# Kernel optimization log

Hardware: AMD Instinct MI355X
Metric: run time of the kernel (lower is better)

## Reference

```python
import jax, jax.numpy as jnp
import numpy as np

NUM_NODES = 100000
NUM_EDGES = 1600000
NUM_GRAPHS = 64
D_IN = 128
HID = 256
N_ATTR = 8
D_OUT = 1


def setup_inputs() -> dict:
    key = jax.random.key(0)
    ks = jax.random.split(key, 16)
    x = jax.random.normal(ks[0], (NUM_NODES, D_IN), dtype=jnp.float32)
    edge_index = jax.random.randint(ks[1], (2, NUM_EDGES), 0, NUM_NODES, dtype=jnp.int64)
    batch = jnp.sort(jax.random.randint(ks[2], (NUM_NODES,), 0, NUM_GRAPHS, dtype=jnp.int64))
    graph_attr = jax.random.normal(ks[3], (NUM_GRAPHS, N_ATTR), dtype=jnp.float32)
    def lin(k, fi, fo):
        s = 1.0 / np.sqrt(fi)
        return jax.random.uniform(k, (fi, fo), jnp.float32, -s, s)
    # SAGEConv: lin_l (applied to aggregated neighbors, has bias) + lin_r (root, no bias)
    W1l = lin(ks[4], D_IN, HID); b1 = jnp.zeros((HID,), jnp.float32)
    W1r = lin(ks[5], D_IN, HID)
    W2l = lin(ks[6], HID, HID); b2 = jnp.zeros((HID,), jnp.float32)
    W2r = lin(ks[7], HID, HID)
    Wf1 = lin(ks[8], HID + N_ATTR, HID); bf1 = jnp.zeros((HID,), jnp.float32)
    Wf2 = lin(ks[9], HID, D_OUT); bf2 = jnp.zeros((D_OUT,), jnp.float32)
    return {"x": x, "edge_index": edge_index, "batch": batch, "graph_attr": graph_attr,
            "W1l": W1l, "b1": b1, "W1r": W1r, "W2l": W2l, "b2": b2, "W2r": W2r,
            "Wf1": Wf1, "bf1": bf1, "Wf2": Wf2, "bf2": bf2}


def _mean_agg(h, src, dst, num_segments):
    # gather source features, scatter-mean into destination nodes
    s = jax.ops.segment_sum(h[src], dst, num_segments=num_segments)
    cnt = jax.ops.segment_sum(jnp.ones((src.shape[0], 1), h.dtype), dst, num_segments=num_segments)
    return s / jnp.maximum(cnt, 1.0)


def _sage(h, src, dst, Wl, b, Wr):
    agg = _mean_agg(h, src, dst, h.shape[0])
    return agg @ Wl + b + h @ Wr


def reference(x, edge_index, batch, graph_attr, W1l, b1, W1r, W2l, b2, W2r, Wf1, bf1, Wf2, bf2):
    src, dst = edge_index[0], edge_index[1]
    h = jax.nn.relu(_sage(x, src, dst, W1l, b1, W1r))
    h = _sage(h, src, dst, W2l, b2, W2r)
    # global mean pool over graphs
    gsum = jax.ops.segment_sum(h, batch, num_segments=NUM_GRAPHS)
    gcnt = jax.ops.segment_sum(jnp.ones((h.shape[0], 1), h.dtype), batch, num_segments=NUM_GRAPHS)
    g = gsum / jnp.maximum(gcnt, 1.0)
    g = jnp.concatenate([g, graph_attr.reshape(-1, N_ATTR)], axis=1)
    g = jax.nn.relu(g @ Wf1 + bf1)
    return g @ Wf2 + bf2
```

## Files before the change

### kernel.cpp

```cpp
#include <hip/hip_runtime.h>
#include <stdint.h>

#define NN 100000
#define NE 1600000
#define NG 64
#define DIN 128
#define HID 256
#define NATTR 8
#define NBK 391
#define CAP 6144
#define PCH 4096
#define BWW 25000
#define CB 12756
#define AEL 2048

typedef unsigned short u16;
typedef __attribute__((ext_vector_type(8))) short s16x8;
typedef __attribute__((ext_vector_type(4))) float f32x4;
typedef __attribute__((ext_vector_type(2))) float f32x2;

__device__ __forceinline__ int imaxi(int a, int b) { return a > b ? a : b; }
__device__ __forceinline__ u16 f2bf(float f) {
    unsigned u = __float_as_uint(f);
    return (u16)((u + 0x7fffu + ((u >> 16) & 1u)) >> 16);
}
__device__ __forceinline__ void gload16(const void* g, void* l) {
    __builtin_amdgcn_global_load_lds((const __attribute__((address_space(1))) void*)g,
                                     (__attribute__((address_space(3))) void*)l, 16, 0, 0);
}


__global__ void k_prep(const float4* __restrict__ x4, ushort4* __restrict__ xb4,
                       const float* __restrict__ W1l, const float* __restrict__ W1r,
                       u16* __restrict__ W1lt, u16* __restrict__ W1rt,
                       float4* __restrict__ P84, const int* __restrict__ batch,
                       int* __restrict__ goff, int* __restrict__ gcnt,
                       int* __restrict__ cursor) {
    int b = blockIdx.x, t = threadIdx.x;
    if (b < CB) {
        int i = b * 256 + t;
        const int NX4 = NN * DIN / 4;
        if (i < NX4) {
            float4 v = x4[i];
            ushort4 o;
            o.x = f2bf(v.x); o.y = f2bf(v.y); o.z = f2bf(v.z); o.w = f2bf(v.w);
            xb4[i] = o;
        } else {
            int j = i - NX4;
            if (j < 32768) {
                int n = j >> 7, k = j & 127;
                W1lt[j] = f2bf(W1l[k * HID + n]);
            } else if (j < 65536) {
                int jj = j - 32768;
                int n = jj >> 7, k = jj & 127;
                W1rt[jj] = f2bf(W1r[k * HID + n]);
            }
        }
    } else if (b < CB + 256) {
        int i = (b - CB) * 256 + t;
        P84[i] = make_float4(0.f, 0.f, 0.f, 0.f);
    } else {
        for (int i = t; i < NBK; i += 256) cursor[i] = 0;
        int g = t;
        if (g <= NG) {
            int lo = 0, hi = NN;
            while (lo < hi) {
                int mid = (lo + hi) >> 1;
                if (batch[mid] < g) lo = mid + 1; else hi = mid;
            }
            goff[g] = lo;
        }
        __syncthreads();
        if (g < NG) gcnt[g] = goff[g + 1] - goff[g];
    }
}


__global__ __launch_bounds__(256) void k_part(const int* __restrict__ ei,
                                              int* __restrict__ cursor,
                                              unsigned* __restrict__ pairs) {
    __shared__ unsigned spk[PCH];
    __shared__ unsigned short sbk[PCH];
    __shared__ int hist[NBK], gb[NBK];
    __shared__ int sc[512];
    int t = threadIdx.x;
    int c0 = blockIdx.x * PCH;
    int n = NE - c0; if (n > PCH) n = PCH;
    for (int i = t; i < NBK; i += 256) hist[i] = 0;
    __syncthreads();
    unsigned mypk[16]; unsigned short mybk[16]; int myoff[16];
#pragma unroll
    for (int j = 0; j < 16; j++) {
        int i = t + j * 256;
        myoff[j] = -1;
        if (i < n) {
            int e = c0 + i;
            unsigned d = (unsigned)__builtin_nontemporal_load(&ei[NE + e]);
            unsigned s = (unsigned)__builtin_nontemporal_load(&ei[e]);
            unsigned bk = d >> 8;
            mypk[j] = ((d & 255u) << 24) | s;
            mybk[j] = (unsigned short)bk;
            myoff[j] = atomicAdd(&hist[bk], 1);
        }
    }
    __syncthreads();
    sc[t] = (t < NBK) ? hist[t] : 0;
    sc[t + 256] = (t + 256 < NBK) ? hist[t + 256] : 0;
    __syncthreads();
    for (int off = 1; off < 512; off <<= 1) {
        int v0 = (t >= off) ? sc[t - off] : 0;
        int v1 = (t + 256 >= off) ? sc[t + 256 - off] : 0;
        __syncthreads();
        sc[t] += v0; sc[t + 256] += v1;
        __syncthreads();
    }
    if (t < NBK && hist[t] > 0) gb[t] = atomicAdd(&cursor[t], hist[t]);
    if (t + 256 < NBK && hist[t + 256] > 0)
        gb[t + 256] = atomicAdd(&cursor[t + 256], hist[t + 256]);
    __syncthreads();
#pragma unroll
    for (int j = 0; j < 16; j++) {
        if (myoff[j] >= 0) {
            int bk = mybk[j];
            int pos = sc[bk] - hist[bk] + myoff[j];
            spk[pos] = mypk[j];
            sbk[pos] = (unsigned short)bk;
        }
    }
    __syncthreads();
    for (int i = t; i < n; i += 256) {
        int bk = sbk[i];
        int local = gb[bk] + (i - (sc[bk] - hist[bk]));
        pairs[(size_t)bk * CAP + local] = spk[i];
    }
}


__global__ __launch_bounds__(256) void k_csr(const unsigned* __restrict__ pairs,
                                             const int* __restrict__ cursor,
                                             int* __restrict__ rowptr,
                                             unsigned* __restrict__ col) {
    __shared__ unsigned colL[CAP];
    __shared__ int csc[512];
    __shared__ int cnt[256], cur[256], sc[256];
    int b = blockIdx.x, t = threadIdx.x;
    csc[t] = (t < NBK) ? cursor[t] : 0;
    csc[t + 256] = (t + 256 < NBK) ? cursor[t + 256] : 0;
    __syncthreads();
    for (int off = 1; off < 512; off <<= 1) {
        int v0 = (t >= off) ? csc[t - off] : 0;
        int v1 = (t + 256 >= off) ? csc[t + 256 - off] : 0;
        __syncthreads();
        csc[t] += v0; csc[t + 256] += v1;
        __syncthreads();
    }
    int obase = (b == 0) ? 0 : csc[b - 1];
    int ecnt = cursor[b];
    const unsigned* pp = pairs + (size_t)b * CAP;
    cnt[t] = 0;
    __syncthreads();
    for (int i = t; i < ecnt; i += 256)
        atomicAdd(&cnt[pp[i] >> 24], 1);
    __syncthreads();
    sc[t] = cnt[t];
    __syncthreads();
    for (int off = 1; off < 256; off <<= 1) {
        int v = (t >= off) ? sc[t - off] : 0;
        __syncthreads();
        sc[t] += v;
        __syncthreads();
    }
    int lr = sc[t] - cnt[t];
    cur[t] = lr;
    int node = (b << 8) + t;
    if (node < NN) rowptr[node] = obase + lr;
    if (b == NBK - 1 && t == 0) rowptr[NN] = obase + ecnt;
    __syncthreads();
    for (int i = t; i < ecnt; i += 256) {
        unsigned p = pp[i];
        int dl = p >> 24;
        int pos = atomicAdd(&cur[dl], 1);
        int dd = cnt[dl]; if (dd > 32767) dd = 32767;
        colL[pos] = ((unsigned)dd << 17) | (p & 0xFFFFFFu);
    }
    __syncthreads();
    for (int i = t; i < ecnt; i += 256)
        col[obase + i] = colL[i];
}


__global__ __launch_bounds__(256, 8) void k_agg(const uint4* __restrict__ xb4,
                                                uint4* __restrict__ agg4,
                                                const int* __restrict__ rowptr,
                                                const unsigned* __restrict__ col,
                                                int node0) {
    __shared__ unsigned scol[AEL];
    int t = threadIdx.x;
    int base = node0 + blockIdx.x * 16;
    int wave = t >> 6, lane = t & 63;
    int qtr = lane >> 4, li = lane & 15;
    int node = base + (wave << 2) + qtr;
    int s = rowptr[node], e = rowptr[node + 1];
    int bs = rowptr[base], be = rowptr[base + 16];
    int bn = be - bs;
    bool inl = bn <= AEL;
    if (inl)
        for (int j = t; j < bn; j += 256) scol[j] = col[bs + j];
    __syncthreads();

    f32x2 b01 = {0.f, 0.f}, b23 = {0.f, 0.f}, b45 = {0.f, 0.f}, b67 = {0.f, 0.f};
    const uint4* xp = xb4 + li;

#define ACC8(V) do { \
        f32x2 p; \
        p[0] = __uint_as_float((V).x << 16); p[1] = __uint_as_float((V).x & 0xffff0000u); b01 += p; \
        p[0] = __uint_as_float((V).y << 16); p[1] = __uint_as_float((V).y & 0xffff0000u); b23 += p; \
        p[0] = __uint_as_float((V).z << 16); p[1] = __uint_as_float((V).z & 0xffff0000u); b45 += p; \
        p[0] = __uint_as_float((V).w << 16); p[1] = __uint_as_float((V).w & 0xffff0000u); b67 += p; \
    } while (0)

#define CL(X) scol[(X) - bs]
#define CG(X) col[X]
#define AGG_BODY(CIDX) do { \
        for (; i + 8 <= e; i += 8) { \
            unsigned c0 = (CIDX(i + 0)) & 0x1FFFFu; \
            unsigned c1 = (CIDX(i + 1)) & 0x1FFFFu; \
            unsigned c2 = (CIDX(i + 2)) & 0x1FFFFu; \
            unsigned c3 = (CIDX(i + 3)) & 0x1FFFFu; \
            unsigned c4 = (CIDX(i + 4)) & 0x1FFFFu; \
            unsigned c5 = (CIDX(i + 5)) & 0x1FFFFu; \
            unsigned c6 = (CIDX(i + 6)) & 0x1FFFFu; \
            unsigned c7 = (CIDX(i + 7)) & 0x1FFFFu; \
            uint4 w0 = xp[(size_t)c0 * 16]; \
            uint4 w1 = xp[(size_t)c1 * 16]; \
            uint4 w2 = xp[(size_t)c2 * 16]; \
            uint4 w3 = xp[(size_t)c3 * 16]; \
            uint4 w4 = xp[(size_t)c4 * 16]; \
            uint4 w5 = xp[(size_t)c5 * 16]; \
            uint4 w6 = xp[(size_t)c6 * 16]; \
            uint4 w7 = xp[(size_t)c7 * 16]; \
            ACC8(w0); ACC8(w1); ACC8(w2); ACC8(w3); \
            ACC8(w4); ACC8(w5); ACC8(w6); ACC8(w7); \
        } \
        for (; i + 2 <= e; i += 2) { \
            unsigned c0 = (CIDX(i + 0)) & 0x1FFFFu; \
            unsigned c1 = (CIDX(i + 1)) & 0x1FFFFu; \
            uint4 w0 = xp[(size_t)c0 * 16]; \
            uint4 w1 = xp[(size_t)c1 * 16]; \
            ACC8(w0); ACC8(w1); \
        } \
        if (i < e) { \
            unsigned c0 = (CIDX(i)) & 0x1FFFFu; \
            uint4 w0 = xp[(size_t)c0 * 16]; \
            ACC8(w0); \
        } \
    } while (0)

    int i = s;
    if (inl) { AGG_BODY(CL); } else { AGG_BODY(CG); }
#undef AGG_BODY
#undef CL
#undef CG
#undef ACC8

    float inv = 1.f / (float)imaxi(e - s, 1);
    uint4 o;
    o.x = (((unsigned)f2bf(b01[1] * inv)) << 16) | (unsigned)f2bf(b01[0] * inv);
    o.y = (((unsigned)f2bf(b23[1] * inv)) << 16) | (unsigned)f2bf(b23[0] * inv);
    o.z = (((unsigned)f2bf(b45[1] * inv)) << 16) | (unsigned)f2bf(b45[0] * inv);
    o.w = (((unsigned)f2bf(b67[1] * inv)) << 16) | (unsigned)f2bf(b67[0] * inv);
    agg4[(size_t)node * 16 + li] = o;
}


__global__ __launch_bounds__(512) void k_gemm1(
    const u16* __restrict__ agg1, const u16* __restrict__ xb,
    const u16* __restrict__ W1lt, const u16* __restrict__ W1rt,
    const float* __restrict__ b1, u16* __restrict__ h1t) {
    __shared__ u16 As[128][32];
    __shared__ u16 Bs[256][32];
    int t = threadIdx.x;
    int m0 = blockIdx.x * 128;
    int wave = t >> 6, lane = t & 63;
    int wm = wave & 1, wn = wave >> 1;
    int lm = lane & 15, quad = lane >> 4;
    int ar = t >> 2, aq = t & 3;
    f32x4 acc[4][4] = {};
    const u16* Ap = agg1;
    const u16* Bp = W1lt;
#pragma unroll
    for (int ph = 0; ph < 2; ph++) {
        for (int k0 = 0; k0 < DIN; k0 += 32) {
            gload16(Ap + (size_t)(m0 + ar) * DIN + k0 + aq * 8, &As[wave * 16][0]);
#pragma unroll
            for (int i = 0; i < 2; i++) {
                int r = (t + i * 512) >> 2;
                gload16(Bp + (size_t)r * DIN + k0 + aq * 8, &Bs[wave * 16 + i * 128][0]);
            }
            __syncthreads();
            s16x8 af[4], bfr[4];
#pragma unroll
            for (int i = 0; i < 4; i++) {
                af[i]  = *(const s16x8*)&As[wm * 64 + i * 16 + lm][quad * 8];
                bfr[i] = *(const s16x8*)&Bs[wn * 64 + i * 16 + lm][quad * 8];
            }
#pragma unroll
            for (int mi = 0; mi < 4; mi++)
#pragma unroll
                for (int ni = 0; ni < 4; ni++)
                    acc[mi][ni] = __builtin_amdgcn_mfma_f32_16x16x32_bf16(
                        af[mi], bfr[ni], acc[mi][ni], 0, 0, 0);
            __syncthreads();
        }
        Ap = xb; Bp = W1rt;
    }
#pragma unroll
    for (int ni = 0; ni < 4; ni++) {
        int colf = wn * 64 + ni * 16 + lm;
        float bias = b1[colf];
#pragma unroll
        for (int mi = 0; mi < 4; mi++) {
            int row = m0 + wm * 64 + mi * 16 + quad * 4;
            if (row < NN) {
                ushort4 o;
                o.x = f2bf(fmaxf(acc[mi][ni][0] + bias, 0.f));
                o.y = f2bf(fmaxf(acc[mi][ni][1] + bias, 0.f));
                o.z = f2bf(fmaxf(acc[mi][ni][2] + bias, 0.f));
                o.w = f2bf(fmaxf(acc[mi][ni][3] + bias, 0.f));
                *(ushort4*)(h1t + (size_t)colf * NN + row) = o;
            }
        }
    }
}


__global__ __launch_bounds__(256) void k_bw(
    const int* __restrict__ rowptr, const unsigned* __restrict__ col,
    const int* __restrict__ goff, u16* __restrict__ Wbt) {
    int b = blockIdx.x, t = threadIdx.x;
    if (b < 256) {
        __shared__ float bins[BWW];
        int g = b >> 2, w = b & 3;
        int lo = w * BWW;
        for (int i = t; i < BWW; i += 256) bins[i] = 0.f;
        __syncthreads();
        int ebeg = rowptr[goff[g]], eend = rowptr[goff[g + 1]];
        for (int i = ebeg + t; i < eend; i += 256) {
            unsigned c = col[i];
            unsigned sl = (c & 0x1FFFFu) - lo;
            if (sl < (unsigned)BWW) atomicAdd(&bins[sl], 1.0f / (float)(c >> 17));
        }
        __syncthreads();
        u16* out = Wbt + (size_t)g * NN + lo;
        for (int k = t; k < BWW / 4; k += 256) {
            ushort4 o;
            o.x = f2bf(bins[4 * k + 0]); o.y = f2bf(bins[4 * k + 1]);
            o.z = f2bf(bins[4 * k + 2]); o.w = f2bf(bins[4 * k + 3]);
            *(ushort4*)(out + 4 * k) = o;
        }
    } else {
        int g = b - 256;
        int a = goff[g], bnd = goff[g + 1];
        u16* out = Wbt + (size_t)(NG + g) * NN;
        for (int k = t; k < NN / 4; k += 256) {
            int c0 = 4 * k;
            ushort4 o;
            o.x = (c0 + 0 >= a && c0 + 0 < bnd) ? 0x3F80 : 0;
            o.y = (c0 + 1 >= a && c0 + 1 < bnd) ? 0x3F80 : 0;
            o.z = (c0 + 2 >= a && c0 + 2 < bnd) ? 0x3F80 : 0;
            o.w = (c0 + 3 >= a && c0 + 3 < bnd) ? 0x3F80 : 0;
            *(ushort4*)(out + c0) = o;
        }
    }
}


#define KCHUNK 512

__global__ __launch_bounds__(512) void k_poolg(
    const u16* __restrict__ Wbt, const u16* __restrict__ h1t, float* __restrict__ P8) {
    __shared__ u16 As[128][32];
    __shared__ u16 Bs[256][32];
    int t = threadIdx.x;
    int kbase = blockIdx.x * KCHUNK;
    int krem = NN - kbase;
    int ksteps = (krem < KCHUNK ? krem : KCHUNK) >> 5;
    int wave = t >> 6, lane = t & 63;
    int wm = wave & 1, wn = wave >> 1;
    int lm = lane & 15, quad = lane >> 4;
    int ar = t >> 2, aq = t & 3;
    float* P = P8 + (size_t)(blockIdx.x & 7) * 128 * HID;
    f32x4 acc[4][4] = {};
    for (int ks = 0; ks < ksteps; ks++) {
        int k0 = kbase + ks * 32;
        gload16(Wbt + (size_t)ar * NN + k0 + aq * 8, &As[wave * 16][0]);
#pragma unroll
        for (int i = 0; i < 2; i++) {
            int r = (t + i * 512) >> 2;
            gload16(h1t + (size_t)r * NN + k0 + aq * 8, &Bs[wave * 16 + i * 128][0]);
        }
        __syncthreads();
        s16x8 af[4], bfr[4];
#pragma unroll
        for (int i = 0; i < 4; i++) {
            af[i]  = *(const s16x8*)&As[wm * 64 + i * 16 + lm][quad * 8];
            bfr[i] = *(const s16x8*)&Bs[wn * 64 + i * 16 + lm][quad * 8];
        }
#pragma unroll
        for (int mi = 0; mi < 4; mi++)
#pragma unroll
            for (int ni = 0; ni < 4; ni++)
                acc[mi][ni] = __builtin_amdgcn_mfma_f32_16x16x32_bf16(
                    af[mi], bfr[ni], acc[mi][ni], 0, 0, 0);
        __syncthreads();
    }
#pragma unroll
    for (int mi = 0; mi < 4; mi++)
#pragma unroll
        for (int ni = 0; ni < 4; ni++) {
            int gcol = wm * 64 + mi * 16 + quad * 4;
            int feat = wn * 64 + ni * 16 + lm;
#pragma unroll
            for (int r = 0; r < 4; r++)
                atomicAdd(&P[(gcol + r) * HID + feat], acc[mi][ni][r]);
        }
}


__global__ void k_head(const float* __restrict__ P8, const int* __restrict__ gcnt,
                       const float* __restrict__ gattr,
                       const float* __restrict__ W2l, const float* __restrict__ b2,
                       const float* __restrict__ W2r,
                       const float* __restrict__ Wf1, const float* __restrict__ bf1,
                       const float* __restrict__ Wf2, const float* __restrict__ bf2v,
                       float* __restrict__ out) {
    __shared__ float pa[HID], ph[HID], gv[HID + NATTR];
    __shared__ float red[256];
    int g = blockIdx.x, t = threadIdx.x;
    float sa = 0.f, sh = 0.f;
#pragma unroll
    for (int c = 0; c < 8; c++) {
        sa += P8[(size_t)c * 128 * HID + g * HID + t];
        sh += P8[(size_t)c * 128 * HID + (NG + g) * HID + t];
    }
    pa[t] = sa; ph[t] = sh;
    __syncthreads();
    float s = 0.f;
    for (int k = 0; k < HID; k++)
        s += pa[k] * W2l[k * HID + t] + ph[k] * W2r[k * HID + t];
    float invc = 1.f / (float)imaxi(gcnt[g], 1);
    gv[t] = s * invc + b2[t];
    if (t < NATTR) gv[HID + t] = gattr[g * NATTR + t];
    __syncthreads();
    float h = bf1[t];
    for (int k = 0; k < HID + NATTR; k++) h += gv[k] * Wf1[k * HID + t];
    h = fmaxf(h, 0.f);
    red[t] = h * Wf2[t];
    __syncthreads();
    for (int off = 128; off > 0; off >>= 1) {
        if (t < off) red[t] += red[t + off];
        __syncthreads();
    }
    if (t == 0) out[g] = red[0] + bf2v[0];
}


extern "C" void kernel_launch(void* const* d_in, const int* in_sizes, int n_in,
                              void* d_out, int out_size, void* d_ws, size_t ws_size,
                              hipStream_t stream) {
    (void)in_sizes; (void)n_in; (void)out_size; (void)ws_size;
    const float* x     = (const float*)d_in[0];
    const int*   ei    = (const int*)d_in[1];
    const int*   batch = (const int*)d_in[2];
    const float* gattr = (const float*)d_in[3];
    const float* W1l   = (const float*)d_in[4];
    const float* b1    = (const float*)d_in[5];
    const float* W1r   = (const float*)d_in[6];
    const float* W2l   = (const float*)d_in[7];
    const float* b2    = (const float*)d_in[8];
    const float* W2r   = (const float*)d_in[9];
    const float* Wf1   = (const float*)d_in[10];
    const float* bf1   = (const float*)d_in[11];
    const float* Wf2   = (const float*)d_in[12];
    const float* bf2v  = (const float*)d_in[13];
    float* out = (float*)d_out;

    uint8_t* w = (uint8_t*)d_ws;
    size_t off = 0;
    auto alloc = [&](size_t bytes) -> void* {
        void* p = w + off;
        off += (bytes + 255) & ~(size_t)255;
        return p;
    };
    u16*      xb     = (u16*)alloc((size_t)NN * DIN * 2);
    u16*      agg1   = (u16*)alloc((size_t)NN * DIN * 2);
    u16*      h1t    = (u16*)alloc((size_t)NN * HID * 2);
    u16*      Wbt    = (u16*)alloc((size_t)128 * NN * 2);
    u16*      W1lt   = (u16*)alloc((size_t)HID * DIN * 2);
    u16*      W1rt   = (u16*)alloc((size_t)HID * DIN * 2);
    unsigned* pairs  = (unsigned*)alloc((size_t)NBK * CAP * 4);
    int*      rowptr = (int*)alloc((size_t)(NN + 1) * 4);
    unsigned* col    = (unsigned*)alloc((size_t)NE * 4);
    int*      cursor = (int*)alloc((NBK + 1) * 4);
    int*      goff   = (int*)alloc((NG + 1) * 4);
    int*      gcnt   = (int*)alloc(NG * 4);
    float*    P8     = (float*)alloc((size_t)8 * 128 * HID * 4);

    k_prep<<<CB + 257, 256, 0, stream>>>((const float4*)x, (ushort4*)xb, W1l, W1r,
                                         W1lt, W1rt, (float4*)P8, batch, goff, gcnt,
                                         cursor);

    k_part<<<(NE + PCH - 1) / PCH, 256, 0, stream>>>(ei, cursor, pairs);
    k_csr<<<NBK, 256, 0, stream>>>(pairs, cursor, rowptr, col);

    k_agg<<<NN / 32, 256, 0, stream>>>((const uint4*)xb, (uint4*)agg1, rowptr, col, 0);
    k_agg<<<NN / 32, 256, 0, stream>>>((const uint4*)xb, (uint4*)agg1, rowptr, col, NN / 2);

    k_gemm1<<<(NN + 127) / 128, 512, 0, stream>>>(agg1, xb, W1lt, W1rt, b1, h1t);

    k_bw<<<320, 256, 0, stream>>>(rowptr, col, goff, Wbt);
    k_poolg<<<(NN + KCHUNK - 1) / KCHUNK, 512, 0, stream>>>(Wbt, h1t, P8);

    k_head<<<NG, 256, 0, stream>>>(P8, gcnt, gattr, W2l, b2, W2r, Wf1, bf1, Wf2, bf2v, out);
}
```

Baseline: 364.5 us.

## Replace per-graph LDS binning with edge-parallel global atomics for pooling weights

The old k_bw used 256 blocks, one per graph quarter, and each block scanned all of that graph's edges to accumulate weights into a 25000-entry LDS histogram. That work was serialized over each graph's edge range and left much of the GPU idle. The new path zeroes a float buffer aliased onto agg1, then scatters edge weights with global atomics across edge-parallel blocks, finding each edge's graph by binary search over graph edge offsets. A separate elementwise kernel converts the buffer to bf16 and writes the indicator rows. This adds two launches, about 25MB of zeroing and float write/read traffic, and contended global atomics, and it reuses agg1 memory after gemm1.

After: 415.5 us. 1.14x slower.

```diff
diff --git a/kernel.cpp b/kernel.cpp
--- a/kernel.cpp
+++ b/kernel.cpp
@@ -10,9 +10,9 @@
 #define NBK 391
 #define CAP 6144
 #define PCH 4096
-#define BWW 25000
 #define CB 12756
 #define AEL 2048
+#define EPB 2048
 
 typedef unsigned short u16;
 typedef __attribute__((ext_vector_type(8))) short s16x8;
@@ -334,43 +334,57 @@
 }
 
 
-__global__ __launch_bounds__(256) void k_bw(
-    const int* __restrict__ rowptr, const unsigned* __restrict__ col,
-    const int* __restrict__ goff, u16* __restrict__ Wbt) {
+__global__ __launch_bounds__(256) void k_zero(float4* __restrict__ p) {
+    p[blockIdx.x * 256 + threadIdx.x] = make_float4(0.f, 0.f, 0.f, 0.f);
+}
+
+__global__ __launch_bounds__(256) void k_bwa(const int* __restrict__ rowptr,
+                                             const unsigned* __restrict__ col,
+                                             const int* __restrict__ goff,
+                                             float* __restrict__ Wbtf) {
+    __shared__ int er[NG + 1];
+    int t = threadIdx.x;
+    if (t <= NG) er[t] = rowptr[goff[t]];
+    __syncthreads();
+    int e0 = blockIdx.x * EPB;
+    int n = NE - e0; if (n > EPB) n = EPB;
+    for (int i = t; i < n; i += 256) {
+        int e = e0 + i;
+        unsigned c = col[e];
+        int lo = 0, hi = NG - 1;
+        while (lo < hi) {
+            int mid = (lo + hi + 1) >> 1;
+            if (er[mid] <= e) lo = mid; else hi = mid - 1;
+        }
+        float wgt = 1.0f / (float)(c >> 17);
+        atomicAdd(&Wbtf[(size_t)lo * NN + (c & 0x1FFFFu)], wgt);
+    }
+}
+
+#define BWC 6250
+
+__global__ __launch_bounds__(256) void k_bwc(const float4* __restrict__ Wbtf4,
+                                             const int* __restrict__ goff,
+                                             u16* __restrict__ Wbt) {
     int b = blockIdx.x, t = threadIdx.x;
-    if (b < 256) {
-        __shared__ float bins[BWW];
-        int g = b >> 2, w = b & 3;
-        int lo = w * BWW;
-        for (int i = t; i < BWW; i += 256) bins[i] = 0.f;
-        __syncthreads();
-        int ebeg = rowptr[goff[g]], eend = rowptr[goff[g + 1]];
-        for (int i = ebeg + t; i < eend; i += 256) {
-            unsigned c = col[i];
-            unsigned sl = (c & 0x1FFFFu) - lo;
-            if (sl < (unsigned)BWW) atomicAdd(&bins[sl], 1.0f / (float)(c >> 17));
-        }
-        __syncthreads();
-        u16* out = Wbt + (size_t)g * NN + lo;
-        for (int k = t; k < BWW / 4; k += 256) {
-            ushort4 o;
-            o.x = f2bf(bins[4 * k + 0]); o.y = f2bf(bins[4 * k + 1]);
-            o.z = f2bf(bins[4 * k + 2]); o.w = f2bf(bins[4 * k + 3]);
-            *(ushort4*)(out + 4 * k) = o;
-        }
+    const int Q = NN / 4;
+    if (b < BWC) {
+        int idx4 = b * 256 + t;
+        float4 v = Wbtf4[idx4];
+        ushort4 o;
+        o.x = f2bf(v.x); o.y = f2bf(v.y); o.z = f2bf(v.z); o.w = f2bf(v.w);
+        ((ushort4*)Wbt)[idx4] = o;
     } else {
-        int g = b - 256;
+        int idx4 = (b - BWC) * 256 + t;
+        int g = idx4 / Q;
+        int c0 = (idx4 - g * Q) * 4;
         int a = goff[g], bnd = goff[g + 1];
-        u16* out = Wbt + (size_t)(NG + g) * NN;
-        for (int k = t; k < NN / 4; k += 256) {
-            int c0 = 4 * k;
-            ushort4 o;
-            o.x = (c0 + 0 >= a && c0 + 0 < bnd) ? 0x3F80 : 0;
-            o.y = (c0 + 1 >= a && c0 + 1 < bnd) ? 0x3F80 : 0;
-            o.z = (c0 + 2 >= a && c0 + 2 < bnd) ? 0x3F80 : 0;
-            o.w = (c0 + 3 >= a && c0 + 3 < bnd) ? 0x3F80 : 0;
-            *(ushort4*)(out + c0) = o;
-        }
+        ushort4 o;
+        o.x = (c0 + 0 >= a && c0 + 0 < bnd) ? 0x3F80 : 0;
+        o.y = (c0 + 1 >= a && c0 + 1 < bnd) ? 0x3F80 : 0;
+        o.z = (c0 + 2 >= a && c0 + 2 < bnd) ? 0x3F80 : 0;
+        o.w = (c0 + 3 >= a && c0 + 3 < bnd) ? 0x3F80 : 0;
+        *(ushort4*)(Wbt + (size_t)(NG + g) * NN + c0) = o;
     }
 }
 
@@ -506,6 +520,8 @@
     int*      gcnt   = (int*)alloc(NG * 4);
     float*    P8     = (float*)alloc((size_t)8 * 128 * HID * 4);
 
+    float* Wbtf = (float*)agg1;
+
     k_prep<<<CB + 257, 256, 0, stream>>>((const float4*)x, (ushort4*)xb, W1l, W1r,
                                          W1lt, W1rt, (float4*)P8, batch, goff, gcnt,
                                          cursor);
@@ -518,7 +534,10 @@
 
     k_gemm1<<<(NN + 127) / 128, 512, 0, stream>>>(agg1, xb, W1lt, W1rt, b1, h1t);
 
-    k_bw<<<320, 256, 0, stream>>>(rowptr, col, goff, Wbt);
+    k_zero<<<NG * NN / 1024, 256, 0, stream>>>((float4*)Wbtf);
+    k_bwa<<<(NE + EPB - 1) / EPB, 256, 0, stream>>>(rowptr, col, goff, Wbtf);
+    k_bwc<<<2 * BWC, 256, 0, stream>>>((const float4*)Wbtf, goff, Wbt);
+
     k_poolg<<<(NN + KCHUNK - 1) / KCHUNK, 512, 0, stream>>>(Wbt, h1t, P8);
 
     k_head<<<NG, 256, 0, stream>>>(P8, gcnt, gattr, W2l, b2, W2r, Wf1, bf1, Wf2, bf2v, out);
```
